# Performance work log

Hardware: AMD Instinct MI355X
Metric: run time of the kernel (lower is better)

The kernel has to match this reference:

```python
import jax, jax.numpy as jnp
import numpy as np

D = 4096       # embed_dim
H = 16         # num_heads
HD = D // H    # head_dim = 256
MLP_H = int(D * 2.0)  # 8192
L_V = 2048
L_T = 1024
GAMMA = 0.6
NOISE_STD = 0.07
TEMP = 0.05
LN_EPS = 1e-5


def setup_inputs() -> dict:
    key = jax.random.key(0)
    ks = jax.random.split(key, 16)
    s = 0.02
    return {
        "vision_feature": jax.random.normal(ks[0], (L_V, D), jnp.float32),
        "text_embed": jax.random.normal(ks[1], (L_T, D), jnp.float32),
        "attention_mask": jnp.zeros((L_T,), jnp.float32),  # additive mask, 0 = attend
        "noise": jax.random.normal(ks[2], (L_V,), jnp.float32),
        "Wq": jax.random.normal(ks[3], (D, D), jnp.float32) * s,
        "bq": jnp.zeros((D,), jnp.float32),
        "Wk": jax.random.normal(ks[4], (D, D), jnp.float32) * s,
        "bk": jnp.zeros((D,), jnp.float32),
        "Wv": jax.random.normal(ks[5], (D, D), jnp.float32) * s,
        "bv": jnp.zeros((D,), jnp.float32),
        "Wo": jax.random.normal(ks[6], (D, D), jnp.float32) * s,
        "bo": jnp.zeros((D,), jnp.float32),
        "ln_w": jnp.ones((D,), jnp.float32),
        "ln_b": jnp.zeros((D,), jnp.float32),
        "W1": jax.random.normal(ks[7], (MLP_H, D), jnp.float32) * s,
        "b1": jnp.zeros((MLP_H,), jnp.float32),
        "W2": jax.random.normal(ks[8], (1, MLP_H), jnp.float32) * s,
        "b2": jnp.zeros((1,), jnp.float32),
    }


def reference(vision_feature, text_embed, attention_mask, noise,
              Wq, bq, Wk, bk, Wv, bv, Wo, bo, ln_w, ln_b, W1, b1, W2, b2):
    # --- cross attention (vision queries over text keys/values) ---
    q = (vision_feature @ Wq.T + bq).reshape(L_V, H, HD)
    k = (text_embed @ Wk.T + bk).reshape(L_T, H, HD)
    v = (text_embed @ Wv.T + bv).reshape(L_T, H, HD)
    logits = jnp.einsum('qhd,khd->hqk', q, k) / np.float32(np.sqrt(HD))
    logits = logits + attention_mask[None, None, :]  # additive attn_mask
    attn = jax.nn.softmax(logits, axis=-1)
    ctx = jnp.einsum('hqk,khd->qhd', attn, v).reshape(L_V, D)
    attn_out = ctx @ Wo.T + bo
    # --- residual + layernorm ---
    x = vision_feature + attn_out
    mu = jnp.mean(x, axis=-1, keepdims=True)
    var = jnp.mean(jnp.square(x - mu), axis=-1, keepdims=True)
    xn = (x - mu) / jnp.sqrt(var + LN_EPS) * ln_w + ln_b
    # --- tiny MLP scorer ---
    h = jax.nn.gelu(xn @ W1.T + b1, approximate=False)
    weight_scores = (h @ W2.T + b2)[:, 0] + noise * NOISE_STD
    # --- temperature softmax over all tokens, top-p (gamma) selection ---
    p = jax.nn.softmax(weight_scores / TEMP, axis=0)
    order = jnp.argsort(-p)           # descending sort indices
    cum = jnp.cumsum(p[order])
    keep = cum <= GAMMA               # threshold_index prefix mask
    gathered = vision_feature[order]  # [L_V, D]
    # fixed-shape stand-in for indices[:threshold_index] gather:
    # valid selected rows are the nonzero prefix
    return jnp.where(keep[:, None], gathered, jnp.zeros((), gathered.dtype))
```

## Files before the change

### kernel.cpp

```cpp
#include <hip/hip_runtime.h>
#include <math.h>


#define LV   2048
#define LT   1024
#define DIM  4096
#define NHD  16
#define HDD  256
#define MLPH 8192

typedef __attribute__((ext_vector_type(8))) short bfx8;
typedef __attribute__((ext_vector_type(4))) float fx4;
typedef unsigned short u16;

__device__ __forceinline__ float wave_sum(float v){
#pragma unroll
  for (int o = 32; o > 0; o >>= 1) v += __shfl_xor(v, o);
  return v;
}
__device__ __forceinline__ float wave_max(float v){
#pragma unroll
  for (int o = 32; o > 0; o >>= 1) v = fmaxf(v, __shfl_xor(v, o));
  return v;
}

__device__ __forceinline__ void splitpack(const float4 a, const float4 b,
                                          bfx8* hi, bfx8* lo){
  float f[8] = {a.x,a.y,a.z,a.w, b.x,b.y,b.z,b.w};
  union { bfx8 v; unsigned u[4]; } H, L;
#pragma unroll
  for (int p = 0; p < 4; ++p){
    unsigned u0 = __float_as_uint(f[2*p]);
    unsigned u1 = __float_as_uint(f[2*p+1]);
    H.u[p] = (u0 >> 16) | (u1 & 0xffff0000u);
    float h0 = __uint_as_float(u0 & 0xffff0000u);
    float h1 = __uint_as_float(u1 & 0xffff0000u);
    unsigned v0 = __float_as_uint(f[2*p]   - h0);
    unsigned v1 = __float_as_uint(f[2*p+1] - h1);
    L.u[p] = (v0 >> 16) | (v1 & 0xffff0000u);
  }
  *hi = H.v; *lo = L.v;
}

__device__ __forceinline__ void glds16(const void* g, void* l){
  __builtin_amdgcn_global_load_lds(
      (const __attribute__((address_space(1))) unsigned int*)g,
      (__attribute__((address_space(3))) unsigned int*)l, 16, 0, 0);
}

__global__ __launch_bounds__(256)
void repack_kernel(const float* __restrict__ src, u16* __restrict__ hi,
                   u16* __restrict__ lo, int Kc, int ktsh)
{
  const long long e = ((long long)blockIdx.x * 256 + threadIdx.x) * 8;
  const int T = (int)(e >> 9);
  const int L = (int)(e >> 3) & 63;
  const int rt = T >> ktsh, kt = T & ((1 << ktsh) - 1);
  const int r = (rt << 4) + (L & 15);
  const int k = (kt << 5) + ((L >> 4) << 3);
  const float* p = src + (long long)r * Kc + k;
  bfx8 h, l;
  splitpack(*(const float4*)p, *(const float4*)(p + 4), &h, &l);
  *(bfx8*)(hi + e) = h;
  *(bfx8*)(lo + e) = l;
}

template<int GELU, int TRANSC>
__global__ __launch_bounds__(256)
void mgemm(const u16* __restrict__ Ah, const u16* __restrict__ Al, int aKT, long long aZe,
           const u16* __restrict__ Bh, const u16* __restrict__ Bl, int bKT, long long bZe,
           float* __restrict__ C, int ldc, long long cZe,
           const float* __restrict__ bias,
           int nx, int KT, int kt0, int zkt, float alpha)
{
  __shared__ bfx8 lbuf[2][32][64];
  const int tid  = threadIdx.x;
  const int lane = tid & 63;
  const int wv   = tid >> 6;
  const int wr   = wv >> 1, wc = wv & 1;
  const int nwg  = gridDim.x;
  const int id   = blockIdx.x;
  const int swz  = (id & 7) * (nwg >> 3) + (id >> 3);
  const int m0   = (swz / nx) << 7;
  const int n0   = (swz % nx) << 7;
  const int z    = blockIdx.z;
  const u16* Ahz = Ah + (long long)z * aZe;
  const u16* Alz = Al + (long long)z * aZe;
  const u16* Bhz = Bh + (long long)z * bZe;
  const u16* Blz = Bl + (long long)z * bZe;
  C += (long long)z * cZe;
  const int ktb  = kt0 + z * zkt;
  const int rtA0 = m0 >> 4, rtB0 = n0 >> 4;

  const fx4 zz = {0.f, 0.f, 0.f, 0.f};
  fx4 acc[4][4];
#pragma unroll
  for (int i = 0; i < 4; ++i)
#pragma unroll
    for (int j = 0; j < 4; ++j) acc[i][j] = zz;

  const u16* wbase = (wv == 0) ? Ahz : (wv == 1) ? Alz : (wv == 2) ? Bhz : Blz;
  const int  wrt0  = (wv < 2) ? rtA0 : rtB0;
  const int  wKT   = (wv < 2) ? aKT  : bKT;

#define STAGE(BUF, KTI)                                                        \
  {                                                                            \
    _Pragma("unroll")                                                          \
    for (int q = 0; q < 8; ++q){                                               \
      const u16* g = wbase + ((long long)(wrt0 + q) * wKT + (KTI)) * 512       \
                     + lane * 8;                                               \
      glds16((const void*)g, (void*)&lbuf[BUF][wv * 8 + q][0]);                \
    }                                                                          \
  }

  int cur = 0;
  STAGE(0, ktb);
  for (int t = 0; t < KT; ++t){
    __syncthreads();
    if (t + 1 < KT) STAGE(cur ^ 1, ktb + t + 1);
    bfx8 ah[4], al[4], bh[4], bl[4];
#pragma unroll
    for (int i = 0; i < 4; ++i){
      ah[i] = lbuf[cur][     wr*4 + i][lane];
      al[i] = lbuf[cur][ 8 + wr*4 + i][lane];
      bh[i] = lbuf[cur][16 + wc*4 + i][lane];
      bl[i] = lbuf[cur][24 + wc*4 + i][lane];
    }
#pragma unroll
    for (int i = 0; i < 4; ++i)
#pragma unroll
      for (int j = 0; j < 4; ++j){
        acc[i][j] = __builtin_amdgcn_mfma_f32_16x16x32_bf16(ah[i], bl[j], acc[i][j], 0, 0, 0);
        acc[i][j] = __builtin_amdgcn_mfma_f32_16x16x32_bf16(al[i], bh[j], acc[i][j], 0, 0, 0);
        acc[i][j] = __builtin_amdgcn_mfma_f32_16x16x32_bf16(ah[i], bh[j], acc[i][j], 0, 0, 0);
      }
    cur ^= 1;
  }
#undef STAGE

#pragma unroll
  for (int i = 0; i < 4; ++i){
    const int row0 = m0 + wr*64 + i*16 + ((lane >> 4) << 2);
#pragma unroll
    for (int j = 0; j < 4; ++j){
      const int col = n0 + wc*64 + j*16 + (lane & 15);
      const float bb = bias ? bias[col] : 0.0f;
      if (TRANSC){
        float4 o;
        o.x = alpha*acc[i][j][0] + bb;
        o.y = alpha*acc[i][j][1] + bb;
        o.z = alpha*acc[i][j][2] + bb;
        o.w = alpha*acc[i][j][3] + bb;
        *(float4*)(C + (size_t)col*ldc + row0) = o;
      } else {
#pragma unroll
        for (int r = 0; r < 4; ++r){
          float v = alpha*acc[i][j][r] + bb;
          if (GELU) v = 0.5f*v*(1.0f + erff(v*0.70710678f));
          C[(size_t)(row0 + r)*ldc + col] = v;
        }
      }
    }
  }
}

template<int GELU, int TRANSC>
__global__ __launch_bounds__(256)
void mgemm_fb(const float* __restrict__ A, long long aZ, int lda,
              const float* __restrict__ B, long long bZ, int ldb,
              float* __restrict__ C, long long cZ, int ldc,
              const float* __restrict__ bias, int Kd, float alpha)
{
  __shared__ bfx8 AhS[512], AlS[512], BhS[512], BlS[512];
  const int tid  = threadIdx.x;
  const int lane = tid & 63;
  const int wv   = tid >> 6;
  const int wr   = wv >> 1, wc = wv & 1;
  const int m0 = blockIdx.y * 128, n0 = blockIdx.x * 128;
  A += (long long)blockIdx.z * aZ;
  B += (long long)blockIdx.z * bZ;
  C += (long long)blockIdx.z * cZ;

  const fx4 zz = {0.f, 0.f, 0.f, 0.f};
  fx4 acc[4][4];
#pragma unroll
  for (int i = 0; i < 4; ++i)
#pragma unroll
    for (int j = 0; j < 4; ++j) acc[i][j] = zz;

  for (int k0 = 0; k0 < Kd; k0 += 32){
    __syncthreads();
#pragma unroll
    for (int pass = 0; pass < 2; ++pass){
      const int s = pass*256 + tid;
      const int m = ((s >> 6) << 4) + (s & 15);
      const int j = (s >> 4) & 3;
      const float* pA = A + (size_t)(m0 + m)*lda + k0 + j*8;
      splitpack(*(const float4*)pA, *(const float4*)(pA + 4), &AhS[s], &AlS[s]);
      const float* pB = B + (size_t)(n0 + m)*ldb + k0 + j*8;
      splitpack(*(const float4*)pB, *(const float4*)(pB + 4), &BhS[s], &BlS[s]);
    }
    __syncthreads();
    bfx8 ah[4], al[4], bh[4], bl[4];
#pragma unroll
    for (int i = 0; i < 4; ++i){
      ah[i] = AhS[(wr*4 + i)*64 + lane];
      al[i] = AlS[(wr*4 + i)*64 + lane];
      bh[i] = BhS[(wc*4 + i)*64 + lane];
      bl[i] = BlS[(wc*4 + i)*64 + lane];
    }
#pragma unroll
    for (int i = 0; i < 4; ++i)
#pragma unroll
      for (int j = 0; j < 4; ++j){
        acc[i][j] = __builtin_amdgcn_mfma_f32_16x16x32_bf16(ah[i], bl[j], acc[i][j], 0, 0, 0);
        acc[i][j] = __builtin_amdgcn_mfma_f32_16x16x32_bf16(al[i], bh[j], acc[i][j], 0, 0, 0);
        acc[i][j] = __builtin_amdgcn_mfma_f32_16x16x32_bf16(ah[i], bh[j], acc[i][j], 0, 0, 0);
      }
  }
#pragma unroll
  for (int i = 0; i < 4; ++i){
    const int row0 = m0 + wr*64 + i*16 + ((lane >> 4) << 2);
#pragma unroll
    for (int j = 0; j < 4; ++j){
      const int col = n0 + wc*64 + j*16 + (lane & 15);
      const float bb = bias ? bias[col] : 0.0f;
      if (TRANSC){
        float4 o;
        o.x = alpha*acc[i][j][0] + bb;
        o.y = alpha*acc[i][j][1] + bb;
        o.z = alpha*acc[i][j][2] + bb;
        o.w = alpha*acc[i][j][3] + bb;
        *(float4*)(C + (size_t)col*ldc + row0) = o;
      } else {
#pragma unroll
        for (int r = 0; r < 4; ++r){
          float v = alpha*acc[i][j][r] + bb;
          if (GELU) v = 0.5f*v*(1.0f + erff(v*0.70710678f));
          C[(size_t)(row0 + r)*ldc + col] = v;
        }
      }
    }
  }
}

__global__ __launch_bounds__(128)
void softmax_pack(const float* __restrict__ Lf, u16* __restrict__ ph,
                  u16* __restrict__ pl)
{
  __shared__ float rr[4];
  const int tid = threadIdx.x;
  const int h = blockIdx.x >> 11;
  const int m = blockIdx.x & 2047;
  const float* row = Lf + ((long long)h * 2048 + m) * 1024;
  const int k = tid * 8;
  float4 a = *(const float4*)(row + k);
  float4 b = *(const float4*)(row + k + 4);
  float v[8] = {a.x,a.y,a.z,a.w, b.x,b.y,b.z,b.w};
  float mx = v[0];
#pragma unroll
  for (int i = 1; i < 8; ++i) mx = fmaxf(mx, v[i]);
  mx = wave_max(mx);
  if ((tid & 63) == 0) rr[tid >> 6] = mx;
  __syncthreads();
  const float M = fmaxf(rr[0], rr[1]);
  float e[8], s = 0.0f;
#pragma unroll
  for (int i = 0; i < 8; ++i){ e[i] = expf(v[i] - M); s += e[i]; }
  s = wave_sum(s);
  if ((tid & 63) == 0) rr[2 + (tid >> 6)] = s;
  __syncthreads();
  const float S = rr[2] + rr[3];
  float4 p0 = make_float4(e[0]/S, e[1]/S, e[2]/S, e[3]/S);
  float4 p1 = make_float4(e[4]/S, e[5]/S, e[6]/S, e[7]/S);
  bfx8 hh, ll;
  splitpack(p0, p1, &hh, &ll);
  const int tile = (m >> 4) * 32 + (k >> 5);
  const int Lw = ((k >> 3) & 3) * 16 + (m & 15);
  const long long eoff = (long long)h * (2048ll*1024) + (long long)tile * 512 + Lw * 8;
  *(bfx8*)(ph + eoff) = hh;
  *(bfx8*)(pl + eoff) = ll;
}

__global__ __launch_bounds__(256)
void softmax_fb(float* __restrict__ X)
{
  __shared__ float r[8];
  const int tid = threadIdx.x;
  float* row = X + (size_t)blockIdx.x * 1024;
  float4 v = ((const float4*)row)[tid];
  float m = fmaxf(fmaxf(v.x,v.y), fmaxf(v.z,v.w));
  m = wave_max(m);
  if ((tid & 63) == 0) r[tid >> 6] = m;
  __syncthreads();
  m = fmaxf(fmaxf(r[0],r[1]), fmaxf(r[2],r[3]));
  float e0 = expf(v.x - m), e1 = expf(v.y - m), e2 = expf(v.z - m), e3 = expf(v.w - m);
  float s = (e0 + e1) + (e2 + e3);
  s = wave_sum(s);
  if ((tid & 63) == 0) r[4 + (tid >> 6)] = s;
  __syncthreads();
  s = (r[4] + r[5]) + (r[6] + r[7]);
  ((float4*)row)[tid] = make_float4(e0/s, e1/s, e2/s, e3/s);
}

template<int PACK>
__global__ __launch_bounds__(256)
void ln_kernel(const float* __restrict__ vis, const float* ao, float* xnf,
               u16* __restrict__ xh, u16* __restrict__ xl,
               const float* __restrict__ w, const float* __restrict__ b)
{
  __shared__ float r[8];
  __shared__ float stat[2];
  const int tid = threadIdx.x;
  const int m = blockIdx.x;
  const size_t base = (size_t)m * DIM + tid * 16;
  float x[16];
#pragma unroll
  for (int q = 0; q < 4; ++q){
    float4 a = *(const float4*)(vis + base + q*4);
    float4 c = *(const float4*)(ao  + base + q*4);
    x[q*4+0]=a.x+c.x; x[q*4+1]=a.y+c.y; x[q*4+2]=a.z+c.z; x[q*4+3]=a.w+c.w;
  }
  float s = 0.0f;
#pragma unroll
  for (int i = 0; i < 16; ++i) s += x[i];
  s = wave_sum(s);
  if ((tid & 63) == 0) r[tid >> 6] = s;
  __syncthreads();
  if (tid == 0) stat[0] = (r[0]+r[1]+r[2]+r[3]) * (1.0f/4096.0f);
  __syncthreads();
  const float mu = stat[0];
  float vs = 0.0f;
#pragma unroll
  for (int i = 0; i < 16; ++i){ float d = x[i]-mu; vs += d*d; }
  vs = wave_sum(vs);
  if ((tid & 63) == 0) r[4 + (tid >> 6)] = vs;
  __syncthreads();
  if (tid == 0) stat[1] = (r[4]+r[5]+r[6]+r[7]) * (1.0f/4096.0f);
  __syncthreads();
  const float inv = 1.0f / sqrtf(stat[1] + 1e-5f);
  const int col = tid * 16;
  float o[16];
#pragma unroll
  for (int q = 0; q < 4; ++q){
    float4 wv = *(const float4*)(w + col + q*4);
    float4 bv = *(const float4*)(b + col + q*4);
    o[q*4+0] = (x[q*4+0]-mu)*inv*wv.x + bv.x;
    o[q*4+1] = (x[q*4+1]-mu)*inv*wv.y + bv.y;
    o[q*4+2] = (x[q*4+2]-mu)*inv*wv.z + bv.z;
    o[q*4+3] = (x[q*4+3]-mu)*inv*wv.w + bv.w;
  }
  if (PACK){
#pragma unroll
    for (int q = 0; q < 2; ++q){
      const int k = col + q*8;
      float4 p0 = make_float4(o[q*8+0], o[q*8+1], o[q*8+2], o[q*8+3]);
      float4 p1 = make_float4(o[q*8+4], o[q*8+5], o[q*8+6], o[q*8+7]);
      bfx8 hh, ll;
      splitpack(p0, p1, &hh, &ll);
      const int tile = (m >> 4) * 128 + (k >> 5);
      const int Lw = ((k >> 3) & 3) * 16 + (m & 15);
      const long long e = (long long)tile * 512 + Lw * 8;
      *(bfx8*)(xh + e) = hh;
      *(bfx8*)(xl + e) = ll;
    }
  } else {
#pragma unroll
    for (int q = 0; q < 4; ++q)
      *(float4*)(xnf + base + q*4) = make_float4(o[q*4+0],o[q*4+1],o[q*4+2],o[q*4+3]);
  }
}

__global__ __launch_bounds__(256)
void score_kernel(const float* __restrict__ H1, const float* __restrict__ W2v,
                  const float* __restrict__ b2, const float* __restrict__ noise,
                  float* __restrict__ sc)
{
  __shared__ float r[4];
  const int tid = threadIdx.x;
  const float* h = H1 + (size_t)blockIdx.x * MLPH + tid * 32;
  const float* w = W2v + tid * 32;
  float s = 0.0f;
#pragma unroll
  for (int q = 0; q < 8; ++q){
    float4 a = *(const float4*)(h + q*4);
    float4 c = *(const float4*)(w + q*4);
    s += a.x*c.x + a.y*c.y + a.z*c.z + a.w*c.w;
  }
  s = wave_sum(s);
  if ((tid & 63) == 0) r[tid >> 6] = s;
  __syncthreads();
  if (tid == 0) sc[blockIdx.x] = (r[0]+r[1]+r[2]+r[3]) + b2[0] + noise[blockIdx.x]*0.07f;
}

__global__ __launch_bounds__(256)
void select_kernel(const float* __restrict__ scores,
                   int* __restrict__ ord, int* __restrict__ kcount)
{
  __shared__ float sv[LV];
  __shared__ int   si[LV];
  __shared__ float red[8];
  const int tid = threadIdx.x;
  for (int i = tid; i < LV; i += 256){ sv[i] = scores[i] / 0.05f; si[i] = i; }
  __syncthreads();
  float m = -3.4e38f;
  for (int i = tid; i < LV; i += 256) m = fmaxf(m, sv[i]);
  m = wave_max(m);
  if ((tid & 63) == 0) red[tid >> 6] = m;
  __syncthreads();
  const float ymax = fmaxf(fmaxf(red[0],red[1]), fmaxf(red[2],red[3]));
  float d = 0.0f;
  for (int i = tid; i < LV; i += 256) d += expf(sv[i] - ymax);
  d = wave_sum(d);
  if ((tid & 63) == 0) red[4 + (tid >> 6)] = d;
  __syncthreads();
  const float denom = (red[4]+red[5]) + (red[6]+red[7]);
  for (int size = 2; size <= LV; size <<= 1){
    for (int stride = size >> 1; stride > 0; stride >>= 1){
      __syncthreads();
      for (int t = tid; t < LV/2; t += 256){
        int i = 2*t - (t & (stride - 1));
        int j = i + stride;
        bool up = ((i & size) == 0);
        float a = sv[i], b = sv[j];
        if ((a < b) == up){
          sv[i] = b; sv[j] = a;
          int ti = si[i]; si[i] = si[j]; si[j] = ti;
        }
      }
    }
  }
  __syncthreads();
  for (int i = tid; i < LV; i += 256) sv[i] = expf(sv[i] - ymax) / denom;
  __syncthreads();
  if (tid == 0){
    float c = 0.0f; int kc = LV;
    for (int j = 0; j < LV; ++j){
      c += sv[j];
      if (!((double)c <= 0.6)){ kc = j; break; }
    }
    *kcount = kc;
  }
  __syncthreads();
  for (int i = tid; i < LV; i += 256) ord[i] = si[i];
}

__global__ __launch_bounds__(256)
void writer_kernel(const float* __restrict__ vis, const int* __restrict__ ord,
                   const int* __restrict__ kc, float* __restrict__ out)
{
  const int j = blockIdx.x;
  float4* dst = (float4*)(out + (size_t)j * DIM);
  if (j < kc[0]){
    const float4* src = (const float4*)(vis + (size_t)ord[j] * DIM);
    for (int i = threadIdx.x; i < DIM/4; i += 256) dst[i] = src[i];
  } else {
    const float4 z4 = make_float4(0.f,0.f,0.f,0.f);
    for (int i = threadIdx.x; i < DIM/4; i += 256) dst[i] = z4;
  }
}

extern "C" void kernel_launch(void* const* d_in, const int* in_sizes, int n_in,
                              void* d_out, int out_size, void* d_ws, size_t ws_size,
                              hipStream_t stream)
{
  (void)in_sizes; (void)n_in; (void)out_size;
  const float* vis  = (const float*)d_in[0];
  const float* txt  = (const float*)d_in[1];
  const float* mask = (const float*)d_in[2];
  const float* noise= (const float*)d_in[3];
  const float* Wq = (const float*)d_in[4];  const float* bq = (const float*)d_in[5];
  const float* Wk = (const float*)d_in[6];  const float* bk = (const float*)d_in[7];
  const float* Wv = (const float*)d_in[8];  const float* bv = (const float*)d_in[9];
  const float* Wo = (const float*)d_in[10]; const float* bo = (const float*)d_in[11];
  const float* lw = (const float*)d_in[12]; const float* lb = (const float*)d_in[13];
  const float* W1 = (const float*)d_in[14]; const float* b1 = (const float*)d_in[15];
  const float* W2 = (const float*)d_in[16]; const float* b2 = (const float*)d_in[17];
  float* out = (float*)d_out;
  const dim3 blk(256);
  const size_t MiB = 1u << 20;

  int Hc = 0;
  for (int h = 16; h >= 1; h >>= 1){
    size_t need = (192 + 16 * (size_t)h) * MiB;
    if (need <= ws_size){ Hc = h; break; }
  }

  if (Hc > 0){
    char* B0 = (char*)d_ws;
    u16* WSh  = (u16*)(B0 + 0);          u16* WSl  = (u16*)(B0 + 32*MiB);
    float* TMPf = (float*)(B0 + 64*MiB);
    u16* QCh  = (u16*)(B0 + 96*MiB);     u16* QCl  = (u16*)(B0 + 112*MiB);
    u16* VCh  = (u16*)(B0 + 128*MiB);    u16* VCl  = (u16*)(B0 + 144*MiB);
    u16* TCh  = (u16*)(B0 + 160*MiB);    u16* TCl  = (u16*)(B0 + 168*MiB);
    float* KF  = (float*)(B0 + 176*MiB);
    float* VTF = (float*)(B0 + 192*MiB);
    u16* VTCh = (u16*)(B0 + 176*MiB);    u16* VTCl = (u16*)(B0 + 184*MiB);
    float* Lf  = (float*)(B0 + 192*MiB);
    u16* PCh  = (u16*)(B0 + (192 + (size_t)Hc*8)*MiB);
    u16* PCl  = (u16*)(B0 + (192 + (size_t)Hc*12)*MiB);
    float* H1f = (float*)(B0 + 128*MiB);
    u16* XNh  = (u16*)(B0 + 96*MiB);     u16* XNl  = (u16*)(B0 + 112*MiB);
    float* SCf = (float*)(B0 + 192*MiB);
    int* ORD = (int*)(SCf + LV);
    int* KCp = ORD + LV;

    repack_kernel<<<dim3(4096), blk, 0, stream>>>(vis, VCh, VCl, 4096, 7);
    repack_kernel<<<dim3(2048), blk, 0, stream>>>(txt, TCh, TCl, 4096, 7);
    repack_kernel<<<dim3(8192), blk, 0, stream>>>(Wq, WSh, WSl, 4096, 7);
    mgemm<0,0><<<dim3(512,1,1), blk, 0, stream>>>(VCh, VCl, 128, 0, WSh, WSl, 128, 0,
        TMPf, 4096, 0, bq, 32, 128, 0, 0, 1.0f);
    repack_kernel<<<dim3(8192), blk, 0, stream>>>(Wk, WSh, WSl, 4096, 7);
    mgemm<0,0><<<dim3(256,1,1), blk, 0, stream>>>(TCh, TCl, 128, 0, WSh, WSl, 128, 0,
        KF, 4096, 0, bk, 32, 128, 0, 0, 1.0f);
    repack_kernel<<<dim3(8192), blk, 0, stream>>>(Wv, WSh, WSl, 4096, 7);
    mgemm<0,1><<<dim3(256,1,1), blk, 0, stream>>>(TCh, TCl, 128, 0, WSh, WSl, 128, 0,
        VTF, 1024, 0, bv, 32, 128, 0, 0, 1.0f);
    repack_kernel<<<dim3(4096), blk, 0, stream>>>(TMPf, QCh, QCl, 4096, 7);
    repack_kernel<<<dim3(2048), blk, 0, stream>>>(KF, TCh, TCl, 4096, 7);
    repack_kernel<<<dim3(2048), blk, 0, stream>>>(VTF, VTCh, VTCl, 1024, 5);
    const int NG = NHD / Hc;
    for (int g = 0; g < NG; ++g){
      mgemm<0,0><<<dim3(128,1,Hc), blk, 0, stream>>>(QCh, QCl, 128, 0, TCh, TCl, 128, 0,
          Lf, 1024, 2097152ll, mask, 8, 8, g*Hc*8, 8, 0.0625f);
      softmax_pack<<<dim3(Hc*2048), dim3(128), 0, stream>>>(Lf, PCh, PCl);
      mgemm<0,0><<<dim3(32,1,Hc), blk, 0, stream>>>(PCh, PCl, 32, 2097152ll,
          VTCh, VTCl, 32, 262144ll,
          TMPf + (long long)g*Hc*256, 4096, 256, nullptr, 2, 32, 0, 0, 1.0f);
    }
    repack_kernel<<<dim3(4096), blk, 0, stream>>>(TMPf, VCh, VCl, 4096, 7);
    repack_kernel<<<dim3(8192), blk, 0, stream>>>(Wo, WSh, WSl, 4096, 7);
    mgemm<0,0><<<dim3(512,1,1), blk, 0, stream>>>(VCh, VCl, 128, 0, WSh, WSl, 128, 0,
        TMPf, 4096, 0, bo, 32, 128, 0, 0, 1.0f);
    ln_kernel<1><<<dim3(LV), blk, 0, stream>>>(vis, TMPf, nullptr, XNh, XNl, lw, lb);
    repack_kernel<<<dim3(8192), blk, 0, stream>>>(W1, WSh, WSl, 4096, 7);
    mgemm<1,0><<<dim3(512,1,1), blk, 0, stream>>>(XNh, XNl, 128, 0, WSh, WSl, 128, 0,
        H1f, 8192, 0, b1, 32, 128, 0, 0, 1.0f);
    repack_kernel<<<dim3(8192), blk, 0, stream>>>(W1 + 16777216ll, WSh, WSl, 4096, 7);
    mgemm<1,0><<<dim3(512,1,1), blk, 0, stream>>>(XNh, XNl, 128, 0, WSh, WSl, 128, 0,
        H1f + 4096, 8192, 0, b1 + 4096, 32, 128, 0, 0, 1.0f);
    score_kernel<<<dim3(LV), blk, 0, stream>>>(H1f, W2, b2, noise, SCf);
    select_kernel<<<dim3(1), blk, 0, stream>>>(SCf, ORD, KCp);
    writer_kernel<<<dim3(LV), blk, 0, stream>>>(vis, ORD, KCp, out);
    return;
  }

  float* ws = (float*)d_ws;
  const long long OQ  = 0;
  const long long OK_ = (long long)LV * DIM;
  const long long OV  = OK_ + (long long)LT * DIM;
  const long long OC  = OV  + (long long)LT * DIM;
  const long long OL  = OC  + (long long)LV * DIM;
  const long long LSTRIDE = (long long)LV * LT;
  int Hf = 16;
  while (Hf > 1){
    size_t need = (size_t)(OL + (long long)Hf * LSTRIDE + 8192) * 4;
    if (need <= ws_size) break;
    Hf >>= 1;
  }
  float* Qw  = ws + OQ;
  float* Kw  = ws + OK_;
  float* Vt  = ws + OV;
  float* Cw  = ws + OC;
  float* Lw  = ws + OL;
  float* H1w = ws + OK_;
  float* SCw = ws + OL + (long long)Hf * LSTRIDE;
  int*   ORDw = (int*)(SCw + LV);
  int*   KCw  = ORDw + LV;

  mgemm_fb<0,0><<<dim3(DIM/128, LV/128, 1), blk, 0, stream>>>(vis,0,DIM, Wq,0,DIM, Qw,0,DIM, bq, DIM, 1.0f);
  mgemm_fb<0,0><<<dim3(DIM/128, LT/128, 1), blk, 0, stream>>>(txt,0,DIM, Wk,0,DIM, Kw,0,DIM, bk, DIM, 1.0f);
  mgemm_fb<0,1><<<dim3(DIM/128, LT/128, 1), blk, 0, stream>>>(txt,0,DIM, Wv,0,DIM, Vt,0,LT, bv, DIM, 1.0f);
  for (int g = 0; g < NHD/Hf; ++g){
    const long long ho = (long long)g * Hf * HDD;
    mgemm_fb<0,0><<<dim3(LT/128, LV/128, Hf), blk, 0, stream>>>(
        Qw+ho, HDD, DIM,  Kw+ho, HDD, DIM,  Lw, LSTRIDE, LT,  mask, HDD, 0.0625f);
    softmax_fb<<<dim3(Hf*LV), blk, 0, stream>>>(Lw);
    mgemm_fb<0,0><<<dim3(HDD/128, LV/128, Hf), blk, 0, stream>>>(
        Lw, LSTRIDE, LT,  Vt + (ho*(long long)LT), (long long)HDD*LT, LT,
        Cw+ho, HDD, DIM,  nullptr, LT, 1.0f);
  }
  mgemm_fb<0,0><<<dim3(DIM/128, LV/128, 1), blk, 0, stream>>>(Cw,0,DIM, Wo,0,DIM, Qw,0,DIM, bo, DIM, 1.0f);
  ln_kernel<0><<<dim3(LV), blk, 0, stream>>>(vis, Qw, Qw, nullptr, nullptr, lw, lb);
  mgemm_fb<1,0><<<dim3(MLPH/128, LV/128, 1), blk, 0, stream>>>(Qw,0,DIM, W1,0,DIM, H1w,0,MLPH, b1, DIM, 1.0f);
  score_kernel<<<dim3(LV), blk, 0, stream>>>(H1w, W2, b2, noise, SCw);
  select_kernel<<<dim3(1), blk, 0, stream>>>(SCw, ORDw, KCw);
  writer_kernel<<<dim3(LV), blk, 0, stream>>>(vis, ORDw, KCw, out);
}
```

Measured before the change: 1.466 ms.

## Switch GEMMs to 32x32x16 MFMA with repacked 32-row tiles and unrolled pipeline

The packed bf16 hi/lo layout changes from 16x32 tiles to 32x16 tiles. The main GEMM now issues 32x32x16 MFMA instructions on fx16 accumulators instead of 16x16x32 ones, which cuts the number of LDS fragment reads per output. The double-buffered K loop is unrolled by two with precomputed, incrementing global pointers. The repack, softmax-pack and layernorm-pack writers and all launch tile strides are updated to match the new layout, and the fallback kernel is only moved in the file. Correctness depends on every producer and consumer agreeing on the new layout and on KT being even.

```diff
diff --git a/kernel.cpp b/kernel.cpp
--- a/kernel.cpp
+++ b/kernel.cpp
@@ -11,6 +11,7 @@
 
 typedef __attribute__((ext_vector_type(8))) short bfx8;
 typedef __attribute__((ext_vector_type(4))) float fx4;
+typedef __attribute__((ext_vector_type(16))) float fx16;
 typedef unsigned short u16;
 
 __device__ __forceinline__ float wave_sum(float v){
@@ -56,8 +57,8 @@
   const int T = (int)(e >> 9);
   const int L = (int)(e >> 3) & 63;
   const int rt = T >> ktsh, kt = T & ((1 << ktsh) - 1);
-  const int r = (rt << 4) + (L & 15);
-  const int k = (kt << 5) + ((L >> 4) << 3);
+  const int r = (rt << 5) + (L & 31);
+  const int k = (kt << 4) + ((L >> 5) << 3);
   const float* p = src + (long long)r * Kc + k;
   bfx8 h, l;
   splitpack(*(const float4*)p, *(const float4*)(p + 4), &h, &l);
@@ -90,41 +91,145 @@
   const u16* Blz = Bl + (long long)z * bZe;
   C += (long long)z * cZe;
   const int ktb  = kt0 + z * zkt;
-  const int rtA0 = m0 >> 4, rtB0 = n0 >> 4;
-
-  const fx4 zz = {0.f, 0.f, 0.f, 0.f};
-  fx4 acc[4][4];
-#pragma unroll
-  for (int i = 0; i < 4; ++i)
-#pragma unroll
-    for (int j = 0; j < 4; ++j) acc[i][j] = zz;
+  const int rtA0 = m0 >> 5, rtB0 = n0 >> 5;
+
+  const fx16 zz = {0.f,0.f,0.f,0.f, 0.f,0.f,0.f,0.f,
+                   0.f,0.f,0.f,0.f, 0.f,0.f,0.f,0.f};
+  fx16 acc[2][2];
+#pragma unroll
+  for (int i = 0; i < 2; ++i)
+#pragma unroll
+    for (int j = 0; j < 2; ++j) acc[i][j] = zz;
 
   const u16* wbase = (wv == 0) ? Ahz : (wv == 1) ? Alz : (wv == 2) ? Bhz : Blz;
   const int  wrt0  = (wv < 2) ? rtA0 : rtB0;
   const int  wKT   = (wv < 2) ? aKT  : bKT;
 
-#define STAGE(BUF, KTI)                                                        \
+  const u16* gp[8];
+#pragma unroll
+  for (int q = 0; q < 8; ++q)
+    gp[q] = wbase + ((long long)(wrt0 + (q >> 1)) * wKT + ktb + (q & 1)) * 512
+            + lane * 8;
+
+#define STAGE(BUF)                                                             \
   {                                                                            \
     _Pragma("unroll")                                                          \
     for (int q = 0; q < 8; ++q){                                               \
-      const u16* g = wbase + ((long long)(wrt0 + q) * wKT + (KTI)) * 512       \
-                     + lane * 8;                                               \
-      glds16((const void*)g, (void*)&lbuf[BUF][wv * 8 + q][0]);                \
+      glds16((const void*)gp[q], (void*)&lbuf[BUF][wv * 8 + q][0]);            \
+      gp[q] += 1024;                                                           \
     }                                                                          \
   }
 
-  int cur = 0;
-  STAGE(0, ktb);
-  for (int t = 0; t < KT; ++t){
+#define COMPUTE(BUF)                                                           \
+  {                                                                            \
+    bfx8 ah[2][2], al[2][2], bh[2][2], bl[2][2];                               \
+    _Pragma("unroll")                                                          \
+    for (int i = 0; i < 2; ++i)                                                \
+      _Pragma("unroll")                                                        \
+      for (int kh = 0; kh < 2; ++kh){                                          \
+        ah[i][kh] = lbuf[BUF][     (wr*2 + i)*2 + kh][lane];                   \
+        al[i][kh] = lbuf[BUF][ 8 + (wr*2 + i)*2 + kh][lane];                   \
+        bh[i][kh] = lbuf[BUF][16 + (wc*2 + i)*2 + kh][lane];                   \
+        bl[i][kh] = lbuf[BUF][24 + (wc*2 + i)*2 + kh][lane];                   \
+      }                                                                        \
+    _Pragma("unroll")                                                          \
+    for (int i = 0; i < 2; ++i)                                                \
+      _Pragma("unroll")                                                        \
+      for (int j = 0; j < 2; ++j){                                             \
+        _Pragma("unroll")                                                      \
+        for (int kh = 0; kh < 2; ++kh){                                        \
+          acc[i][j] = __builtin_amdgcn_mfma_f32_32x32x16_bf16(ah[i][kh], bl[j][kh], acc[i][j], 0, 0, 0); \
+          acc[i][j] = __builtin_amdgcn_mfma_f32_32x32x16_bf16(al[i][kh], bh[j][kh], acc[i][j], 0, 0, 0); \
+          acc[i][j] = __builtin_amdgcn_mfma_f32_32x32x16_bf16(ah[i][kh], bh[j][kh], acc[i][j], 0, 0, 0); \
+        }                                                                      \
+      }                                                                        \
+  }
+
+  STAGE(0);
+  for (int t = 0; t < KT; t += 2){
     __syncthreads();
-    if (t + 1 < KT) STAGE(cur ^ 1, ktb + t + 1);
+    STAGE(1);
+    COMPUTE(0);
+    __syncthreads();
+    if (t + 2 < KT) STAGE(0);
+    COMPUTE(1);
+  }
+#undef STAGE
+#undef COMPUTE
+
+#pragma unroll
+  for (int i = 0; i < 2; ++i){
+#pragma unroll
+    for (int j = 0; j < 2; ++j){
+      const int col = n0 + wc*64 + j*32 + (lane & 31);
+      const float bb = bias ? bias[col] : 0.0f;
+#pragma unroll
+      for (int g = 0; g < 4; ++g){
+        const int row0 = m0 + wr*64 + i*32 + g*8 + ((lane >> 5) << 2);
+        if (TRANSC){
+          float4 o;
+          o.x = alpha*acc[i][j][g*4+0] + bb;
+          o.y = alpha*acc[i][j][g*4+1] + bb;
+          o.z = alpha*acc[i][j][g*4+2] + bb;
+          o.w = alpha*acc[i][j][g*4+3] + bb;
+          *(float4*)(C + (size_t)col*ldc + row0) = o;
+        } else {
+#pragma unroll
+          for (int r = 0; r < 4; ++r){
+            float v = alpha*acc[i][j][g*4+r] + bb;
+            if (GELU) v = 0.5f*v*(1.0f + erff(v*0.70710678f));
+            C[(size_t)(row0 + r)*ldc + col] = v;
+          }
+        }
+      }
+    }
+  }
+}
+
+template<int GELU, int TRANSC>
+__global__ __launch_bounds__(256)
+void mgemm_fb(const float* __restrict__ A, long long aZ, int lda,
+              const float* __restrict__ B, long long bZ, int ldb,
+              float* __restrict__ C, long long cZ, int ldc,
+              const float* __restrict__ bias, int Kd, float alpha)
+{
+  __shared__ bfx8 AhS[512], AlS[512], BhS[512], BlS[512];
+  const int tid  = threadIdx.x;
+  const int lane = tid & 63;
+  const int wv   = tid >> 6;
+  const int wr   = wv >> 1, wc = wv & 1;
+  const int m0 = blockIdx.y * 128, n0 = blockIdx.x * 128;
+  A += (long long)blockIdx.z * aZ;
+  B += (long long)blockIdx.z * bZ;
+  C += (long long)blockIdx.z * cZ;
+
+  const fx4 zz = {0.f, 0.f, 0.f, 0.f};
+  fx4 acc[4][4];
+#pragma unroll
+  for (int i = 0; i < 4; ++i)
+#pragma unroll
+    for (int j = 0; j < 4; ++j) acc[i][j] = zz;
+
+  for (int k0 = 0; k0 < Kd; k0 += 32){
+    __syncthreads();
+#pragma unroll
+    for (int pass = 0; pass < 2; ++pass){
+      const int s = pass*256 + tid;
+      const int m = ((s >> 6) << 4) + (s & 15);
+      const int j = (s >> 4) & 3;
+      const float* pA = A + (size_t)(m0 + m)*lda + k0 + j*8;
+      splitpack(*(const float4*)pA, *(const float4*)(pA + 4), &AhS[s], &AlS[s]);
+      const float* pB = B + (size_t)(n0 + m)*ldb + k0 + j*8;
+      splitpack(*(const float4*)pB, *(const float4*)(pB + 4), &BhS[s], &BlS[s]);
+    }
+    __syncthreads();
     bfx8 ah[4], al[4], bh[4], bl[4];
 #pragma unroll
     for (int i = 0; i < 4; ++i){
-      ah[i] = lbuf[cur][     wr*4 + i][lane];
-      al[i] = lbuf[cur][ 8 + wr*4 + i][lane];
-      bh[i] = lbuf[cur][16 + wc*4 + i][lane];
-      bl[i] = lbuf[cur][24 + wc*4 + i][lane];
+      ah[i] = AhS[(wr*4 + i)*64 + lane];
+      al[i] = AlS[(wr*4 + i)*64 + lane];
+      bh[i] = BhS[(wc*4 + i)*64 + lane];
+      bl[i] = BlS[(wc*4 + i)*64 + lane];
     }
 #pragma unroll
     for (int i = 0; i < 4; ++i)
@@ -134,10 +239,7 @@
         acc[i][j] = __builtin_amdgcn_mfma_f32_16x16x32_bf16(al[i], bh[j], acc[i][j], 0, 0, 0);
         acc[i][j] = __builtin_amdgcn_mfma_f32_16x16x32_bf16(ah[i], bh[j], acc[i][j], 0, 0, 0);
       }
-    cur ^= 1;
-  }
-#undef STAGE
-
+  }
 #pragma unroll
   for (int i = 0; i < 4; ++i){
     const int row0 = m0 + wr*64 + i*16 + ((lane >> 4) << 2);
@@ -164,86 +266,6 @@
   }
 }
 
-template<int GELU, int TRANSC>
-__global__ __launch_bounds__(256)
-void mgemm_fb(const float* __restrict__ A, long long aZ, int lda,
-              const float* __restrict__ B, long long bZ, int ldb,
-              float* __restrict__ C, long long cZ, int ldc,
-              const float* __restrict__ bias, int Kd, float alpha)
-{
-  __shared__ bfx8 AhS[512], AlS[512], BhS[512], BlS[512];
-  const int tid  = threadIdx.x;
-  const int lane = tid & 63;
-  const int wv   = tid >> 6;
-  const int wr   = wv >> 1, wc = wv & 1;
-  const int m0 = blockIdx.y * 128, n0 = blockIdx.x * 128;
-  A += (long long)blockIdx.z * aZ;
-  B += (long long)blockIdx.z * bZ;
-  C += (long long)blockIdx.z * cZ;
-
-  const fx4 zz = {0.f, 0.f, 0.f, 0.f};
-  fx4 acc[4][4];
-#pragma unroll
-  for (int i = 0; i < 4; ++i)
-#pragma unroll
-    for (int j = 0; j < 4; ++j) acc[i][j] = zz;
-
-  for (int k0 = 0; k0 < Kd; k0 += 32){
-    __syncthreads();
-#pragma unroll
-    for (int pass = 0; pass < 2; ++pass){
-      const int s = pass*256 + tid;
-      const int m = ((s >> 6) << 4) + (s & 15);
-      const int j = (s >> 4) & 3;
-      const float* pA = A + (size_t)(m0 + m)*lda + k0 + j*8;
-      splitpack(*(const float4*)pA, *(const float4*)(pA + 4), &AhS[s], &AlS[s]);
-      const float* pB = B + (size_t)(n0 + m)*ldb + k0 + j*8;
-      splitpack(*(const float4*)pB, *(const float4*)(pB + 4), &BhS[s], &BlS[s]);
-    }
-    __syncthreads();
-    bfx8 ah[4], al[4], bh[4], bl[4];
-#pragma unroll
-    for (int i = 0; i < 4; ++i){
-      ah[i] = AhS[(wr*4 + i)*64 + lane];
-      al[i] = AlS[(wr*4 + i)*64 + lane];
-      bh[i] = BhS[(wc*4 + i)*64 + lane];
-      bl[i] = BlS[(wc*4 + i)*64 + lane];
-    }
-#pragma unroll
-    for (int i = 0; i < 4; ++i)
-#pragma unroll
-      for (int j = 0; j < 4; ++j){
-        acc[i][j] = __builtin_amdgcn_mfma_f32_16x16x32_bf16(ah[i], bl[j], acc[i][j], 0, 0, 0);
-        acc[i][j] = __builtin_amdgcn_mfma_f32_16x16x32_bf16(al[i], bh[j], acc[i][j], 0, 0, 0);
-        acc[i][j] = __builtin_amdgcn_mfma_f32_16x16x32_bf16(ah[i], bh[j], acc[i][j], 0, 0, 0);
-      }
-  }
-#pragma unroll
-  for (int i = 0; i < 4; ++i){
-    const int row0 = m0 + wr*64 + i*16 + ((lane >> 4) << 2);
-#pragma unroll
-    for (int j = 0; j < 4; ++j){
-      const int col = n0 + wc*64 + j*16 + (lane & 15);
-      const float bb = bias ? bias[col] : 0.0f;
-      if (TRANSC){
-        float4 o;
-        o.x = alpha*acc[i][j][0] + bb;
-        o.y = alpha*acc[i][j][1] + bb;
-        o.z = alpha*acc[i][j][2] + bb;
-        o.w = alpha*acc[i][j][3] + bb;
-        *(float4*)(C + (size_t)col*ldc + row0) = o;
-      } else {
-#pragma unroll
-        for (int r = 0; r < 4; ++r){
-          float v = alpha*acc[i][j][r] + bb;
-          if (GELU) v = 0.5f*v*(1.0f + erff(v*0.70710678f));
-          C[(size_t)(row0 + r)*ldc + col] = v;
-        }
-      }
-    }
-  }
-}
-
 __global__ __launch_bounds__(128)
 void softmax_pack(const float* __restrict__ Lf, u16* __restrict__ ph,
                   u16* __restrict__ pl)
@@ -275,9 +297,9 @@
   float4 p1 = make_float4(e[4]/S, e[5]/S, e[6]/S, e[7]/S);
   bfx8 hh, ll;
   splitpack(p0, p1, &hh, &ll);
-  const int tile = (m >> 4) * 32 + (k >> 5);
-  const int Lw = ((k >> 3) & 3) * 16 + (m & 15);
-  const long long eoff = (long long)h * (2048ll*1024) + (long long)tile * 512 + Lw * 8;
+  const int T = (m >> 5) * 64 + (tid >> 1);
+  const int Lw = (m & 31) + ((tid & 1) << 5);
+  const long long eoff = (long long)h * (2048ll*1024) + (long long)T * 512 + Lw * 8;
   *(bfx8*)(ph + eoff) = hh;
   *(bfx8*)(pl + eoff) = ll;
 }
@@ -358,9 +380,9 @@
       float4 p1 = make_float4(o[q*8+4], o[q*8+5], o[q*8+6], o[q*8+7]);
       bfx8 hh, ll;
       splitpack(p0, p1, &hh, &ll);
-      const int tile = (m >> 4) * 128 + (k >> 5);
-      const int Lw = ((k >> 3) & 3) * 16 + (m & 15);
-      const long long e = (long long)tile * 512 + Lw * 8;
+      const int T = (m >> 5) * 256 + (k >> 4);
+      const int Lw = (m & 31) + (((k >> 3) & 1) << 5);
+      const long long e = (long long)T * 512 + Lw * 8;
       *(bfx8*)(xh + e) = hh;
       *(bfx8*)(xl + e) = ll;
     }
@@ -505,39 +527,39 @@
     int* ORD = (int*)(SCf + LV);
     int* KCp = ORD + LV;
 
-    repack_kernel<<<dim3(4096), blk, 0, stream>>>(vis, VCh, VCl, 4096, 7);
-    repack_kernel<<<dim3(2048), blk, 0, stream>>>(txt, TCh, TCl, 4096, 7);
-    repack_kernel<<<dim3(8192), blk, 0, stream>>>(Wq, WSh, WSl, 4096, 7);
-    mgemm<0,0><<<dim3(512,1,1), blk, 0, stream>>>(VCh, VCl, 128, 0, WSh, WSl, 128, 0,
+    repack_kernel<<<dim3(4096), blk, 0, stream>>>(vis, VCh, VCl, 4096, 8);
+    repack_kernel<<<dim3(2048), blk, 0, stream>>>(txt, TCh, TCl, 4096, 8);
+    repack_kernel<<<dim3(8192), blk, 0, stream>>>(Wq, WSh, WSl, 4096, 8);
+    mgemm<0,0><<<dim3(512,1,1), blk, 0, stream>>>(VCh, VCl, 256, 0, WSh, WSl, 256, 0,
         TMPf, 4096, 0, bq, 32, 128, 0, 0, 1.0f);
-    repack_kernel<<<dim3(8192), blk, 0, stream>>>(Wk, WSh, WSl, 4096, 7);
-    mgemm<0,0><<<dim3(256,1,1), blk, 0, stream>>>(TCh, TCl, 128, 0, WSh, WSl, 128, 0,
+    repack_kernel<<<dim3(8192), blk, 0, stream>>>(Wk, WSh, WSl, 4096, 8);
+    mgemm<0,0><<<dim3(256,1,1), blk, 0, stream>>>(TCh, TCl, 256, 0, WSh, WSl, 256, 0,
         KF, 4096, 0, bk, 32, 128, 0, 0, 1.0f);
-    repack_kernel<<<dim3(8192), blk, 0, stream>>>(Wv, WSh, WSl, 4096, 7);
-    mgemm<0,1><<<dim3(256,1,1), blk, 0, stream>>>(TCh, TCl, 128, 0, WSh, WSl, 128, 0,
+    repack_kernel<<<dim3(8192), blk, 0, stream>>>(Wv, WSh, WSl, 4096, 8);
+    mgemm<0,1><<<dim3(256,1,1), blk, 0, stream>>>(TCh, TCl, 256, 0, WSh, WSl, 256, 0,
         VTF, 1024, 0, bv, 32, 128, 0, 0, 1.0f);
-    repack_kernel<<<dim3(4096), blk, 0, stream>>>(TMPf, QCh, QCl, 4096, 7);
-    repack_kernel<<<dim3(2048), blk, 0, stream>>>(KF, TCh, TCl, 4096, 7);
-    repack_kernel<<<dim3(2048), blk, 0, stream>>>(VTF, VTCh, VTCl, 1024, 5);
+    repack_kernel<<<dim3(4096), blk, 0, stream>>>(TMPf, QCh, QCl, 4096, 8);
+    repack_kernel<<<dim3(2048), blk, 0, stream>>>(KF, TCh, TCl, 4096, 8);
+    repack_kernel<<<dim3(2048), blk, 0, stream>>>(VTF, VTCh, VTCl, 1024, 6);
     const int NG = NHD / Hc;
     for (int g = 0; g < NG; ++g){
-      mgemm<0,0><<<dim3(128,1,Hc), blk, 0, stream>>>(QCh, QCl, 128, 0, TCh, TCl, 128, 0,
-          Lf, 1024, 2097152ll, mask, 8, 8, g*Hc*8, 8, 0.0625f);
+      mgemm<0,0><<<dim3(128,1,Hc), blk, 0, stream>>>(QCh, QCl, 256, 0, TCh, TCl, 256, 0,
+          Lf, 1024, 2097152ll, mask, 8, 8, g*Hc*16, 16, 0.0625f);
       softmax_pack<<<dim3(Hc*2048), dim3(128), 0, stream>>>(Lf, PCh, PCl);
-      mgemm<0,0><<<dim3(32,1,Hc), blk, 0, stream>>>(PCh, PCl, 32, 2097152ll,
-          VTCh, VTCl, 32, 262144ll,
+      mgemm<0,0><<<dim3(32,1,Hc), blk, 0, stream>>>(PCh, PCl, 64, 2097152ll,
+          VTCh + (long long)g*Hc*262144, VTCl + (long long)g*Hc*262144, 64, 262144ll,
           TMPf + (long long)g*Hc*256, 4096, 256, nullptr, 2, 32, 0, 0, 1.0f);
     }
-    repack_kernel<<<dim3(4096), blk, 0, stream>>>(TMPf, VCh, VCl, 4096, 7);
-    repack_kernel<<<dim3(8192), blk, 0, stream>>>(Wo, WSh, WSl, 4096, 7);
-    mgemm<0,0><<<dim3(512,1,1), blk, 0, stream>>>(VCh, VCl, 128, 0, WSh, WSl, 128, 0,
+    repack_kernel<<<dim3(4096), blk, 0, stream>>>(TMPf, VCh, VCl, 4096, 8);
+    repack_kernel<<<dim3(8192), blk, 0, stream>>>(Wo, WSh, WSl, 4096, 8);
+    mgemm<0,0><<<dim3(512,1,1), blk, 0, stream>>>(VCh, VCl, 256, 0, WSh, WSl, 256, 0,
         TMPf, 4096, 0, bo, 32, 128, 0, 0, 1.0f);
     ln_kernel<1><<<dim3(LV), blk, 0, stream>>>(vis, TMPf, nullptr, XNh, XNl, lw, lb);
-    repack_kernel<<<dim3(8192), blk, 0, stream>>>(W1, WSh, WSl, 4096, 7);
-    mgemm<1,0><<<dim3(512,1,1), blk, 0, stream>>>(XNh, XNl, 128, 0, WSh, WSl, 128, 0,
+    repack_kernel<<<dim3(8192), blk, 0, stream>>>(W1, WSh, WSl, 4096, 8);
+    mgemm<1,0><<<dim3(512,1,1), blk, 0, stream>>>(XNh, XNl, 256, 0, WSh, WSl, 256, 0,
         H1f, 8192, 0, b1, 32, 128, 0, 0, 1.0f);
-    repack_kernel<<<dim3(8192), blk, 0, stream>>>(W1 + 16777216ll, WSh, WSl, 4096, 7);
-    mgemm<1,0><<<dim3(512,1,1), blk, 0, stream>>>(XNh, XNl, 128, 0, WSh, WSl, 128, 0,
+    repack_kernel<<<dim3(8192), blk, 0, stream>>>(W1 + 16777216ll, WSh, WSl, 4096, 8);
+    mgemm<1,0><<<dim3(512,1,1), blk, 0, stream>>>(XNh, XNl, 256, 0, WSh, WSl, 256, 0,
         H1f + 4096, 8192, 0, b1 + 4096, 32, 128, 0, 0, 1.0f);
     score_kernel<<<dim3(LV), blk, 0, stream>>>(H1f, W2, b2, noise, SCf);
     select_kernel<<<dim3(1), blk, 0, stream>>>(SCf, ORD, KCp);
```

Result: slower. 1.591 ms (+8.5%).
